# Kernel tuning notes

Hardware: AMD Instinct MI355X
Metric: run time of the kernel (lower is better)

## Reference

```python
import jax, jax.numpy as jnp
import numpy as np

ANCHOR_NUM = 8
CLASS_NUM = 2
IN_DIM = 1024

def setup_inputs() -> dict:
    key = jax.random.key(0)
    k1, k2, k3, k4 = jax.random.split(key, 4)
    batch_input = jax.random.normal(k1, (64, 512, IN_DIM), dtype=jnp.float32)
    # labels in {-1, 0, 1}: -1 = padding, 0 = negative anchor, 1 = positive anchor
    anchor_labels = jax.random.randint(k2, (64, 512, ANCHOR_NUM), 0, 3, dtype=jnp.int64 if jax.config.read('jax_enable_x64') else jnp.int32) - 1
    lim = 1.0 / np.sqrt(IN_DIM)
    W = jax.random.uniform(k3, (IN_DIM, ANCHOR_NUM * CLASS_NUM), dtype=jnp.float32, minval=-lim, maxval=lim)
    b = jax.random.uniform(k4, (ANCHOR_NUM * CLASS_NUM,), dtype=jnp.float32, minval=-lim, maxval=lim)
    return {"batch_input": batch_input, "W": W, "b": b, "anchor_labels": anchor_labels}

def reference(batch_input, W, b, anchor_labels):
    B, S, _ = batch_input.shape
    # logits: (B, S, anchor_num, class_num)
    logits = (jnp.einsum('bsd,dk->bsk', batch_input, W) + b).reshape(B, S, ANCHOR_NUM, CLASS_NUM)
    predict_label = jnp.argmax(logits, axis=3)  # (B, S, A)
    valid = (anchor_labels != -1)
    labels = jnp.maximum(anchor_labels, 0)  # safe class index for padded entries
    logp = jax.nn.log_softmax(logits, axis=-1)
    nll = -jnp.take_along_axis(logp, labels[..., None].astype(jnp.int32), axis=-1)[..., 0]
    # CrossEntropyLoss (mean) over all non-padding anchors == eval-path gather + CE
    vf = valid.astype(logits.dtype)
    loss = jnp.sum(nll * vf) / jnp.maximum(jnp.sum(vf), 1.0)
    # candidate mask stands in for candidate_idx (positive predictions, non-padding)
    candidate_mask = (predict_label == 1) & valid
    return loss, predict_label, candidate_mask
```

## Files before the change

kernel.cpp:

```cpp
#include <hip/hip_runtime.h>
#include <math.h>


#define ROWS   64
#define NW     8
#define KSLICE 128
#define CHUNK  32
#define NCH    (KSLICE/CHUNK)
#define SLABF  (ROWS*CHUNK)
#define RSTR   136

typedef __attribute__((address_space(3))) void       lds_v;
typedef const __attribute__((address_space(1))) void gbl_v;

__device__ __forceinline__ void stage16(const float* g, float* l)
{
    __builtin_amdgcn_global_load_lds((gbl_v*)g, (lds_v*)l, 16, 0, 0);
}

__global__ __launch_bounds__(512, 2)
void rpn_main(const float* __restrict__ x, const float* __restrict__ W,
              const float* __restrict__ b, const int* __restrict__ lab,
              float* __restrict__ out, float* __restrict__ ws)
{
    __shared__ float xs[NW * SLABF];
    float* red = xs;

    const int tid  = threadIdx.x;
    const int lane = tid & 63;
    const int ks   = __builtin_amdgcn_readfirstlane(tid >> 6);
    const int row0 = blockIdx.x * ROWS;

    const int rsub = lane >> 3;
    const int tq   = (lane & 7) ^ rsub;

    float* slab = xs + ks * SLABF;
    const float* gstage = x + (size_t)(row0 + rsub) * 1024 + ks * KSLICE + tq * 4;
    const float* wk     = W + (size_t)(ks * KSLICE) * 16;

    float acc[16];
#pragma unroll
    for (int c = 0; c < 16; ++c) acc[c] = 0.f;

#pragma unroll
    for (int i = 0; i < 8; ++i)
        stage16(gstage + i * 8192, slab + i * 256);

#define FMA16(V, WROW)                                            \
    do {                                                          \
        const float* _w = (WROW);                                 \
        _Pragma("unroll")                                         \
        for (int c = 0; c < 16; ++c)                              \
            acc[c] = fmaf((V), _w[c], acc[c]);                    \
    } while (0)

#pragma unroll 1
    for (int ch = 0; ch < NCH; ++ch) {
        asm volatile("s_waitcnt vmcnt(0)" ::: "memory");
        __builtin_amdgcn_sched_barrier(0);

        float4 xq[8];
#pragma unroll
        for (int t = 0; t < 8; ++t)
            xq[t] = *(const float4*)(slab + lane * 32 + ((t ^ (lane & 7)) << 2));

        asm volatile("s_waitcnt lgkmcnt(0)" ::: "memory");
        __builtin_amdgcn_sched_barrier(0);
        if (ch + 1 < NCH) {
            const float* g = gstage + (ch + 1) * CHUNK;
#pragma unroll
            for (int i = 0; i < 8; ++i)
                stage16(g + i * 8192, slab + i * 256);
        }

        const float* wc = wk + (size_t)(ch * CHUNK) * 16;
#pragma unroll
        for (int t = 0; t < 8; ++t) {
            FMA16(xq[t].x, wc + (t * 4 + 0) * 16);
            FMA16(xq[t].y, wc + (t * 4 + 1) * 16);
            FMA16(xq[t].z, wc + (t * 4 + 2) * 16);
            FMA16(xq[t].w, wc + (t * 4 + 3) * 16);
        }
    }
#undef FMA16

    __syncthreads();
    {
        float* rp = red + lane * RSTR + ks * 16;
        *(float4*)(rp + 0)  = make_float4(acc[0],  acc[1],  acc[2],  acc[3]);
        *(float4*)(rp + 4)  = make_float4(acc[4],  acc[5],  acc[6],  acc[7]);
        *(float4*)(rp + 8)  = make_float4(acc[8],  acc[9],  acc[10], acc[11]);
        *(float4*)(rp + 12) = make_float4(acc[12], acc[13], acc[14], acc[15]);
    }
    __syncthreads();

    if (tid < ROWS) {
        const int row = row0 + tid;
        float L[16];
#pragma unroll
        for (int c = 0; c < 16; ++c) {
            float s = 0.f;
#pragma unroll
            for (int k = 0; k < NW; ++k) s += red[tid * RSTR + k * 16 + c];
            L[c] = s + b[c];
        }

        const int* labp  = lab + (size_t)row * 8;
        float*     predp = out + 1 + (size_t)row * 8;
        float*     maskp = out + 1 + 262144 + (size_t)row * 8;

        float lsum = 0.f, lcnt = 0.f;
#pragma unroll
        for (int a = 0; a < 8; ++a) {
            float l0 = L[2 * a], l1 = L[2 * a + 1];
            int   lb = labp[a];
            int   pred  = (l1 > l0) ? 1 : 0;
            int   valid = (lb != -1);
            float m   = fmaxf(l0, l1);
            float lse = m + logf(expf(l0 - m) + expf(l1 - m));
            float nll = lse - ((lb == 1) ? l1 : l0);
            if (valid) { lsum += nll; lcnt += 1.f; }
            predp[a] = (float)pred;
            maskp[a] = (pred && valid) ? 1.f : 0.f;
        }

#pragma unroll
        for (int off = 32; off > 0; off >>= 1) {
            lsum += __shfl_down(lsum, off, 64);
            lcnt += __shfl_down(lcnt, off, 64);
        }
        if (tid == 0) {
            atomicAdd(&ws[0], lsum);
            atomicAdd(&ws[1], lcnt);
        }
    }
}

__global__ void rpn_final(const float* __restrict__ ws, float* __restrict__ out)
{
    out[0] = ws[0] / fmaxf(ws[1], 1.f);
}

extern "C" void kernel_launch(void* const* d_in, const int* in_sizes, int n_in,
                              void* d_out, int out_size, void* d_ws, size_t ws_size,
                              hipStream_t stream)
{
    const float* x   = (const float*)d_in[0];
    const float* W   = (const float*)d_in[1];
    const float* b   = (const float*)d_in[2];
    const int*   lab = (const int*)d_in[3];
    float* out = (float*)d_out;
    float* ws  = (float*)d_ws;

    hipMemsetAsync(ws, 0, 2 * sizeof(float), stream);
    rpn_main<<<dim3(512), dim3(512), 0, stream>>>(x, W, b, lab, out, ws);
    rpn_final<<<dim3(1), dim3(1), 0, stream>>>(ws, out);
}
```

Baseline: 215.7 us.

## Double-buffer LDS staging with four waves and fold finalize into last block

Each block now runs four waves, each covering a 256-wide K slice over eight chunks. The staging slabs are double-buffered and the wait is vmcnt(8), so the global-to-LDS load of chunk ch+2 overlaps the compute on chunk ch. The separate finalize kernel is replaced by a last-block-done atomic counter that computes the mean loss, removing one launch. The trade-off is half as many waves per block, so less parallelism for hiding latency, and an extra atomic plus threadfence per block.

```diff
diff --git a/kernel.cpp b/kernel.cpp
--- a/kernel.cpp
+++ b/kernel.cpp
@@ -3,12 +3,12 @@
 
 
 #define ROWS   64
-#define NW     8
-#define KSLICE 128
+#define NWAVE  4
+#define KSLICE 256
 #define CHUNK  32
-#define NCH    (KSLICE/CHUNK)
+#define NCH    8
 #define SLABF  (ROWS*CHUNK)
-#define RSTR   136
+#define RSTR   68
 
 typedef __attribute__((address_space(3))) void       lds_v;
 typedef const __attribute__((address_space(1))) void gbl_v;
@@ -18,33 +18,35 @@
     __builtin_amdgcn_global_load_lds((gbl_v*)g, (lds_v*)l, 16, 0, 0);
 }
 
-__global__ __launch_bounds__(512, 2)
+__global__ __launch_bounds__(256, 2)
 void rpn_main(const float* __restrict__ x, const float* __restrict__ W,
               const float* __restrict__ b, const int* __restrict__ lab,
               float* __restrict__ out, float* __restrict__ ws)
 {
-    __shared__ float xs[NW * SLABF];
+    __shared__ float xs[NWAVE * 2 * SLABF];
     float* red = xs;
 
     const int tid  = threadIdx.x;
     const int lane = tid & 63;
-    const int ks   = __builtin_amdgcn_readfirstlane(tid >> 6);
+    const int wv   = __builtin_amdgcn_readfirstlane(tid >> 6);
     const int row0 = blockIdx.x * ROWS;
 
     const int rsub = lane >> 3;
     const int tq   = (lane & 7) ^ rsub;
 
-    float* slab = xs + ks * SLABF;
-    const float* gstage = x + (size_t)(row0 + rsub) * 1024 + ks * KSLICE + tq * 4;
-    const float* wk     = W + (size_t)(ks * KSLICE) * 16;
+    float* slab0 = xs + wv * (2 * SLABF);
+    float* slab1 = slab0 + SLABF;
+    const float* gst = x + (size_t)(row0 + rsub) * 1024 + wv * KSLICE + tq * 4;
+    const float* wk  = W + (size_t)(wv * KSLICE) * 16;
 
     float acc[16];
 #pragma unroll
     for (int c = 0; c < 16; ++c) acc[c] = 0.f;
 
 #pragma unroll
-    for (int i = 0; i < 8; ++i)
-        stage16(gstage + i * 8192, slab + i * 256);
+    for (int i = 0; i < 8; ++i) stage16(gst + i * 8192,         slab0 + i * 256);
+#pragma unroll
+    for (int i = 0; i < 8; ++i) stage16(gst + CHUNK + i * 8192, slab1 + i * 256);
 
 #define FMA16(V, WROW)                                            \
     do {                                                          \
@@ -56,21 +58,27 @@
 
 #pragma unroll 1
     for (int ch = 0; ch < NCH; ++ch) {
-        asm volatile("s_waitcnt vmcnt(0)" ::: "memory");
+        float* cur = (ch & 1) ? slab1 : slab0;
+
+        if (ch == NCH - 1) {
+            asm volatile("s_waitcnt vmcnt(0)" ::: "memory");
+        } else {
+            asm volatile("s_waitcnt vmcnt(8)" ::: "memory");
+        }
         __builtin_amdgcn_sched_barrier(0);
 
         float4 xq[8];
 #pragma unroll
         for (int t = 0; t < 8; ++t)
-            xq[t] = *(const float4*)(slab + lane * 32 + ((t ^ (lane & 7)) << 2));
+            xq[t] = *(const float4*)(cur + lane * 32 + ((t ^ (lane & 7)) << 2));
 
         asm volatile("s_waitcnt lgkmcnt(0)" ::: "memory");
         __builtin_amdgcn_sched_barrier(0);
-        if (ch + 1 < NCH) {
-            const float* g = gstage + (ch + 1) * CHUNK;
+        if (ch + 2 < NCH) {
+            const float* g = gst + (ch + 2) * CHUNK;
 #pragma unroll
             for (int i = 0; i < 8; ++i)
-                stage16(g + i * 8192, slab + i * 256);
+                stage16(g + i * 8192, cur + i * 256);
         }
 
         const float* wc = wk + (size_t)(ch * CHUNK) * 16;
@@ -86,7 +94,7 @@
 
     __syncthreads();
     {
-        float* rp = red + lane * RSTR + ks * 16;
+        float* rp = red + lane * RSTR + wv * 16;
         *(float4*)(rp + 0)  = make_float4(acc[0],  acc[1],  acc[2],  acc[3]);
         *(float4*)(rp + 4)  = make_float4(acc[4],  acc[5],  acc[6],  acc[7]);
         *(float4*)(rp + 8)  = make_float4(acc[8],  acc[9],  acc[10], acc[11]);
@@ -101,7 +109,7 @@
         for (int c = 0; c < 16; ++c) {
             float s = 0.f;
 #pragma unroll
-            for (int k = 0; k < NW; ++k) s += red[tid * RSTR + k * 16 + c];
+            for (int k = 0; k < NWAVE; ++k) s += red[tid * RSTR + k * 16 + c];
             L[c] = s + b[c];
         }
 
@@ -132,13 +140,15 @@
         if (tid == 0) {
             atomicAdd(&ws[0], lsum);
             atomicAdd(&ws[1], lcnt);
+            __threadfence();
+            unsigned int old = atomicAdd((unsigned int*)(ws + 2), 1u);
+            if (old == gridDim.x - 1) {
+                float Sf = atomicAdd(&ws[0], 0.f);
+                float Cf = atomicAdd(&ws[1], 0.f);
+                out[0] = Sf / fmaxf(Cf, 1.f);
+            }
         }
     }
-}
-
-__global__ void rpn_final(const float* __restrict__ ws, float* __restrict__ out)
-{
-    out[0] = ws[0] / fmaxf(ws[1], 1.f);
 }
 
 extern "C" void kernel_launch(void* const* d_in, const int* in_sizes, int n_in,
@@ -152,7 +162,6 @@
     float* out = (float*)d_out;
     float* ws  = (float*)d_ws;
 
-    hipMemsetAsync(ws, 0, 2 * sizeof(float), stream);
-    rpn_main<<<dim3(512), dim3(512), 0, stream>>>(x, W, b, lab, out, ws);
-    rpn_final<<<dim3(1), dim3(1), 0, stream>>>(ws, out);
+    hipMemsetAsync(ws, 0, 16, stream);
+    rpn_main<<<dim3(512), dim3(256), 0, stream>>>(x, W, b, lab, out, ws);
 }
```

Measured after the change: 234.1 us. +8.5%, slower.
